# Performance work log

Measured on AMD Instinct MI355X. Metric: run time of the kernel, lower is better.

The kernel has to match this reference:

```python
import jax, jax.numpy as jnp
import numpy as np

D_MODEL = 256
N_HEADS = 4
WINDOW = 8
DECAY = 0.9
STEP_SIZE = 0.5


def _linear(x, w, b):
    # torch nn.Linear: y = x @ w.T + b, w: [out, in]
    return jnp.einsum('...i,oi->...o', x, w) + b


def _layernorm(x, scale, bias, eps=1e-5):
    mu = jnp.mean(x, axis=-1, keepdims=True)
    var = jnp.var(x, axis=-1, keepdims=True)
    return (x - mu) * jax.lax.rsqrt(var + eps) * scale + bias


def _ema(x, decay):
    # ema[t] = decay*ema[t-1] + (1-decay)*x[t], ema[-1]=0
    # (exactly the causal conv with weights (1-d)*d^i from the torch code)
    def step(c, xt):
        c = decay * c + (1.0 - decay) * xt
        return c, c
    _, ys = jax.lax.scan(step, jnp.zeros_like(x[:, 0]), jnp.swapaxes(x, 0, 1))
    return jnp.swapaxes(ys, 0, 1)


def setup_inputs() -> dict:
    key = jax.random.key(0)
    ks = iter(jax.random.split(key, 40))
    B, T, D = 8, 1024, D_MODEL
    s = 0.02
    inp = {
        'parallel_repr': jax.random.normal(next(ks), (B, T, D), jnp.float32),
        'sequential_state': jax.random.normal(next(ks), (B, D), jnp.float32),
        'trajectory_summary': jax.random.normal(next(ks), (B, D), jnp.float32),
        # MultiheadAttention params
        'in_proj_w': jax.random.normal(next(ks), (3 * D, D), jnp.float32) * s,
        'in_proj_b': jnp.zeros((3 * D,), jnp.float32),
        'out_proj_w': jax.random.normal(next(ks), (D, D), jnp.float32) * s,
        'out_proj_b': jnp.zeros((D,), jnp.float32),
        # depthwise causal conv (local history)
        'conv_w': jax.random.normal(next(ks), (D, 1, WINDOW), jnp.float32) * s,
        'conv_b': jnp.zeros((D,), jnp.float32),
        # parallel_to_sequential / sequential_to_parallel
        'p2s_w': jax.random.normal(next(ks), (D, D), jnp.float32) * s,
        'p2s_b': jnp.zeros((D,), jnp.float32),
        's2p_w': jax.random.normal(next(ks), (D, D), jnp.float32) * s,
        's2p_b': jnp.zeros((D,), jnp.float32),
        # transition MLP: 3D -> 2D -> D
        'trans_w1': jax.random.normal(next(ks), (2 * D, 3 * D), jnp.float32) * s,
        'trans_b1': jnp.zeros((2 * D,), jnp.float32),
        'trans_w2': jax.random.normal(next(ks), (D, 2 * D), jnp.float32) * s,
        'trans_b2': jnp.zeros((D,), jnp.float32),
        # FFN: D -> 4D -> D
        'ffn_w1': jax.random.normal(next(ks), (4 * D, D), jnp.float32) * s,
        'ffn_b1': jnp.zeros((4 * D,), jnp.float32),
        'ffn_w2': jax.random.normal(next(ks), (D, 4 * D), jnp.float32) * s,
        'ffn_b2': jnp.zeros((D,), jnp.float32),
        # LayerNorms
        'ln1_s': jnp.ones((D,), jnp.float32), 'ln1_b': jnp.zeros((D,), jnp.float32),
        'ln2_s': jnp.ones((D,), jnp.float32), 'ln2_b': jnp.zeros((D,), jnp.float32),
        'ln3_s': jnp.ones((D,), jnp.float32), 'ln3_b': jnp.zeros((D,), jnp.float32),
        'ln4_s': jnp.ones((D,), jnp.float32), 'ln4_b': jnp.zeros((D,), jnp.float32),
    }
    return inp


def _forward(parallel_repr, sequential_state,
             in_proj_w, in_proj_b, out_proj_w, out_proj_b,
             conv_w, conv_b, p2s_w, p2s_b, s2p_w, s2p_b,
             trans_w1, trans_b1, trans_w2, trans_b2,
             ffn_w1, ffn_b1, ffn_w2, ffn_b2,
             ln1_s, ln1_b, ln2_s, ln2_b, ln3_s, ln3_b, ln4_s, ln4_b):
    B, T, D = parallel_repr.shape
    H, hd = N_HEADS, D // N_HEADS

    # --- causal self-attention (nn.MultiheadAttention, batch_first) ---
    qkv = _linear(parallel_repr, in_proj_w, in_proj_b)
    q, k, v = jnp.split(qkv, 3, axis=-1)
    q = q.reshape(B, T, H, hd)
    k = k.reshape(B, T, H, hd)
    v = v.reshape(B, T, H, hd)
    scores = jnp.einsum('bqhd,bkhd->bhqk', q, k) / jnp.sqrt(jnp.asarray(hd, q.dtype))
    causal = jnp.triu(jnp.ones((T, T), bool), 1)
    scores = jnp.where(causal, jnp.finfo(scores.dtype).min, scores)
    attn = jax.nn.softmax(scores, axis=-1)
    attn_out = jnp.einsum('bhqk,bkhd->bqhd', attn, v).reshape(B, T, D)
    attn_out = _linear(attn_out, out_proj_w, out_proj_b)
    x = _layernorm(parallel_repr + attn_out, ln1_s, ln1_b)

    # --- depthwise causal conv (local history) ---
    xt = jnp.swapaxes(x, 1, 2)  # [B, D, T]
    xt_pad = jnp.pad(xt, ((0, 0), (0, 0), (WINDOW - 1, 0)))
    local = jax.lax.conv_general_dilated(
        xt_pad, conv_w, window_strides=(1,), padding='VALID',
        dimension_numbers=('NCH', 'OIH', 'NCH'), feature_group_count=D)
    local_history = jnp.swapaxes(local + conv_b[None, :, None], 1, 2)  # [B, T, D]

    # --- global EMA summary ---
    global_summary = _ema(x, DECAY)

    # --- transition deltas + cumsum state integration ---
    parallel_guidance = _linear(x, p2s_w, p2s_b)
    combined = jnp.concatenate([x + 0.3 * parallel_guidance, local_history, global_summary], axis=-1)
    h = jax.nn.gelu(_linear(combined, trans_w1, trans_b1), approximate=False)
    deltas = _linear(h, trans_w2, trans_b2)
    states = sequential_state[:, None, :] + jnp.cumsum(deltas, axis=1) * STEP_SIZE
    states = _layernorm(states, ln3_s, ln3_b)

    # --- FFN with sequential guidance ---
    seq_guidance = _linear(states, s2p_w, s2p_b)
    f = jax.nn.gelu(_linear(x + 0.3 * seq_guidance, ffn_w1, ffn_b1), approximate=False)
    ffn_out = _linear(f, ffn_w2, ffn_b2)
    x = _layernorm(x + ffn_out, ln2_s, ln2_b)

    final_sequential_state = _layernorm(states[:, -1, :], ln4_s, ln4_b)
    final_trajectory_summary = global_summary[:, -1, :]
    return x, final_sequential_state, final_trajectory_summary


def reference(parallel_repr, sequential_state, trajectory_summary,
              in_proj_w, in_proj_b, out_proj_w, out_proj_b,
              conv_w, conv_b, p2s_w, p2s_b, s2p_w, s2p_b,
              trans_w1, trans_b1, trans_w2, trans_b2,
              ffn_w1, ffn_b1, ffn_w2, ffn_b2,
              ln1_s, ln1_b, ln2_s, ln2_b, ln3_s, ln3_b, ln4_s, ln4_b):
    # trajectory_summary is accepted by the torch forward but never used.
    return _forward(parallel_repr, sequential_state,
                    in_proj_w, in_proj_b, out_proj_w, out_proj_b,
                    conv_w, conv_b, p2s_w, p2s_b, s2p_w, s2p_b,
                    trans_w1, trans_b1, trans_w2, trans_b2,
                    ffn_w1, ffn_b1, ffn_w2, ffn_b2,
                    ln1_s, ln1_b, ln2_s, ln2_b, ln3_s, ln3_b, ln4_s, ln4_b)
```

## Files before the change

kernel.cpp:

```cpp
#include <hip/hip_runtime.h>
#include <math.h>

typedef unsigned short u16;
typedef __attribute__((ext_vector_type(8))) short bf16x8;
typedef __attribute__((ext_vector_type(4))) float f32x4;

#define D_MODEL 256
#define T_SZ 1024
constexpr size_t S_ELT = (size_t)8192 * 256;
constexpr size_t MB = 1024 * 1024;

constexpr size_t OFF_QKV = 0;
constexpr size_t OFF_ATTN = 12 * MB;
constexpr size_t OFF_F = 0;
constexpr size_t OFF_X = 16 * MB;
constexpr size_t OFF_COMB = 24 * MB;
constexpr size_t OFF_FB = 36 * MB;
constexpr size_t OFF_H = 44 * MB;
constexpr size_t OFF_WB = 52 * MB;
constexpr size_t OFF_SCR1 = 55 * MB;
constexpr size_t OFF_SCR2 = 55 * MB + 262144;

constexpr int WB_INPROJ = 0;
constexpr int WB_OUTPROJ = 196608;
constexpr int WB_P2S = 262144;
constexpr int WB_S2P = 327680;
constexpr int WB_T1 = 393216;
constexpr int WB_T2 = 786432;
constexpr int WB_F1 = 917504;
constexpr int WB_F2 = 1179648;
constexpr int WB_TOTAL = 1441792;

__device__ __forceinline__ u16 f2bf(float f) {
  unsigned int u = __float_as_uint(f);
  u += 0x7fff + ((u >> 16) & 1);
  return (u16)(u >> 16);
}
__device__ __forceinline__ float bf2f(u16 s) {
  return __uint_as_float(((unsigned int)s) << 16);
}

__global__ __launch_bounds__(256)
void wconv_kernel(const float* w0, const float* w1, const float* w2,
                  const float* w3, const float* w4, const float* w5,
                  const float* w6, const float* w7, u16* __restrict__ outp) {
  const int idx4 = (blockIdx.x * 256 + threadIdx.x) * 4;
  if (idx4 >= WB_TOTAL) return;
  const int offs[9] = {WB_INPROJ, WB_OUTPROJ, WB_P2S,  WB_S2P, WB_T1,
                       WB_T2,     WB_F1,      WB_F2,   WB_TOTAL};
  const float* srcs[8] = {w0, w1, w2, w3, w4, w5, w6, w7};
  int seg = 0;
  while (idx4 >= offs[seg + 1]) ++seg;
  float4 v = *(const float4*)(srcs[seg] + (idx4 - offs[seg]));
  u16 o0 = f2bf(v.x), o1 = f2bf(v.y), o2 = f2bf(v.z), o3 = f2bf(v.w);
  unsigned int lo = (unsigned int)o0 | ((unsigned int)o1 << 16);
  unsigned int hi = (unsigned int)o2 | ((unsigned int)o3 << 16);
  uint2 pk = make_uint2(lo, hi);
  *(uint2*)(outp + idx4) = pk;
}

enum { EPI_NONE = 0, EPI_GELU = 1, EPI_ADDSCALE = 2 };

template <int EPI, int BN, bool OUTBF, bool AF32>
__global__ __launch_bounds__(256)
void mgemm(const void* __restrict__ Av, int lda,
           const u16* __restrict__ Wb, int K, const float* __restrict__ bias,
           void* __restrict__ Cv, int ldc, int col_off,
           const float* __restrict__ addsrc) {
  __shared__ u16 As[128][40];
  __shared__ u16 Bs[BN][40];
  const int tid = threadIdx.x;
  const int m0 = blockIdx.x * 128;
  const int n0 = blockIdx.y * BN;
  const int w = tid >> 6, lane = tid & 63;
  const int ln = lane & 15, quad = lane >> 4, kq8 = quad * 8;
  constexpr int MT = (BN == 128) ? 4 : 2;
  const int wm = (BN == 128) ? (w >> 1) * 64 : w * 32;
  const int wn = (BN == 128) ? (w & 1) * 64 : 0;

  f32x4 acc[MT][4] = {};

  const int srow = tid >> 2, skq = tid & 3;

  for (int k0 = 0; k0 < K; k0 += 32) {
    if (AF32) {
      const float* Af = (const float*)Av;
#pragma unroll
      for (int p = 0; p < 2; ++p) {
        const int row = srow + p * 64;
        const float* ap = Af + (size_t)(m0 + row) * lda + k0 + skq * 8;
        float4 v0 = *(const float4*)ap;
        float4 v1 = *(const float4*)(ap + 4);
        union { u16 h[8]; uint4 u; } pk;
        pk.h[0] = f2bf(v0.x); pk.h[1] = f2bf(v0.y);
        pk.h[2] = f2bf(v0.z); pk.h[3] = f2bf(v0.w);
        pk.h[4] = f2bf(v1.x); pk.h[5] = f2bf(v1.y);
        pk.h[6] = f2bf(v1.z); pk.h[7] = f2bf(v1.w);
        *(uint4*)&As[row][skq * 8] = pk.u;
      }
    } else {
      const u16* Ab = (const u16*)Av;
#pragma unroll
      for (int p = 0; p < 2; ++p) {
        const int row = srow + p * 64;
        *(uint4*)&As[row][skq * 8] =
            *(const uint4*)(Ab + (size_t)(m0 + row) * lda + k0 + skq * 8);
      }
    }
    *(uint4*)&Bs[srow][skq * 8] =
        *(const uint4*)(Wb + (size_t)(n0 + srow) * K + k0 + skq * 8);
    if (BN == 128) {
      *(uint4*)&Bs[srow + 64][skq * 8] =
          *(const uint4*)(Wb + (size_t)(n0 + srow + 64) * K + k0 + skq * 8);
    }
    __syncthreads();

    bf16x8 af[MT], bv[4];
#pragma unroll
    for (int i = 0; i < MT; ++i)
      af[i] = *(const bf16x8*)&As[wm + i * 16 + ln][kq8];
#pragma unroll
    for (int j = 0; j < 4; ++j)
      bv[j] = *(const bf16x8*)&Bs[wn + j * 16 + ln][kq8];
#pragma unroll
    for (int i = 0; i < MT; ++i)
#pragma unroll
      for (int j = 0; j < 4; ++j)
        acc[i][j] =
            __builtin_amdgcn_mfma_f32_16x16x32_bf16(af[i], bv[j], acc[i][j], 0, 0, 0);
    __syncthreads();
  }

#pragma unroll
  for (int i = 0; i < MT; ++i)
#pragma unroll
    for (int j = 0; j < 4; ++j) {
      const int col = n0 + wn + j * 16 + ln;
      const float bsv = bias[col];
#pragma unroll
      for (int r = 0; r < 4; ++r) {
        const int row = m0 + wm + i * 16 + quad * 4 + r;
        float v = acc[i][j][r] + bsv;
        if (EPI == EPI_GELU) v = 0.5f * v * (1.0f + erff(v * 0.70710678f));
        if (EPI == EPI_ADDSCALE) v = addsrc[(size_t)row * 256 + col] + 0.3f * v;
        if (OUTBF)
          ((u16*)Cv)[(size_t)row * ldc + col_off + col] = f2bf(v);
        else
          ((float*)Cv)[(size_t)row * ldc + col_off + col] = v;
      }
    }
}

__global__ __launch_bounds__(256)
void vtr_kernel(const u16* __restrict__ qkv, u16* __restrict__ vt) {
  __shared__ u16 Ls[64][66];
  const int tid = threadIdx.x;
  const int t0 = blockIdx.x * 64;
  const int bh = blockIdx.y;
  const int b = bh >> 2, h = bh & 3;
  const int r0 = tid >> 3, c8 = (tid & 7) * 8;
#pragma unroll
  for (int p = 0; p < 2; ++p) {
    const int t = t0 + r0 + p * 32;
    *(uint4*)&Ls[r0 + p * 32][c8] =
        *(const uint4*)(qkv + (size_t)(b * T_SZ + t) * 768 + 512 + h * 64 + c8);
  }
  __syncthreads();
#pragma unroll
  for (int p = 0; p < 2; ++p) {
    const int d = r0 + p * 32;
    union { u16 h16[8]; uint4 u; } pk;
#pragma unroll
    for (int e = 0; e < 8; ++e) pk.h16[e] = Ls[c8 + e][d];
    *(uint4*)(vt + (size_t)(bh * 64 + d) * T_SZ + t0 + c8) = pk.u;
  }
}

__global__ __launch_bounds__(256)
void attn_flash(const u16* __restrict__ qkv, const u16* __restrict__ vt,
                u16* __restrict__ outp) {
  __shared__ u16 Ps[4][16][72];
  const int tid = threadIdx.x;
  const int w = tid >> 6, lane = tid & 63;
  const int ln = lane & 15, quad = lane >> 4, kq8 = quad * 8;
  const int wu = blockIdx.x * 4 + w;
  const int bh = wu >> 6, s = wu & 63;
  const int qt = (s & 1) ? (63 - (s >> 1)) : (s >> 1);
  const int q0 = qt * 16;
  const int b = bh >> 2, h = bh & 3;
  const u16* base = qkv + (size_t)b * T_SZ * 768;
  const u16* vbase = vt + (size_t)bh * 64 * T_SZ;

  bf16x8 qf[2];
#pragma unroll
  for (int ks = 0; ks < 2; ++ks)
    qf[ks] = *(const bf16x8*)(base + (size_t)(q0 + ln) * 768 + h * 64 +
                              ks * 32 + kq8);
  const short ob = (short)0x3F80;
  const bf16x8 ones = {ob, ob, ob, ob, ob, ob, ob, ob};

  f32x4 O[4] = {};
  f32x4 l_acc = {};
  const int ntiles = (qt >> 2) + 1;
  for (int jt = 0; jt < ntiles; ++jt) {
    const int c0 = jt * 64;
    f32x4 sv[4] = {};
#pragma unroll
    for (int ks = 0; ks < 2; ++ks)
#pragma unroll
      for (int j = 0; j < 4; ++j) {
        bf16x8 kf = *(const bf16x8*)(base + (size_t)(c0 + j * 16 + ln) * 768 +
                                     256 + h * 64 + ks * 32 + kq8);
        sv[j] = __builtin_amdgcn_mfma_f32_16x16x32_bf16(qf[ks], kf, sv[j], 0, 0, 0);
      }
    const bool need_mask = (c0 + 63 > q0);
#pragma unroll
    for (int j = 0; j < 4; ++j)
#pragma unroll
      for (int r = 0; r < 4; ++r) {
        float p = __expf(sv[j][r] * 0.125f);
        if (need_mask && (c0 + j * 16 + ln > q0 + quad * 4 + r)) p = 0.f;
        Ps[w][quad * 4 + r][j * 16 + ln] = f2bf(p);
      }
#pragma unroll
    for (int ks = 0; ks < 2; ++ks) {
      bf16x8 pf = *(const bf16x8*)&Ps[w][ln][ks * 32 + kq8];
      l_acc = __builtin_amdgcn_mfma_f32_16x16x32_bf16(pf, ones, l_acc, 0, 0, 0);
#pragma unroll
      for (int j = 0; j < 4; ++j) {
        bf16x8 vf = *(const bf16x8*)(vbase + (size_t)(j * 16 + ln) * T_SZ +
                                     c0 + ks * 32 + kq8);
        O[j] = __builtin_amdgcn_mfma_f32_16x16x32_bf16(pf, vf, O[j], 0, 0, 0);
      }
    }
  }
  u16* op = outp + (size_t)b * T_SZ * 256;
#pragma unroll
  for (int r = 0; r < 4; ++r) {
    const float inv = 1.f / l_acc[r];
#pragma unroll
    for (int j = 0; j < 4; ++j)
      op[(size_t)(q0 + quad * 4 + r) * 256 + h * 64 + j * 16 + ln] =
          f2bf(O[j][r] * inv);
  }
}

__device__ __forceinline__ float block_reduce_sum(float v, float* tmp) {
#pragma unroll
  for (int o = 32; o > 0; o >>= 1) v += __shfl_down(v, o);
  const int lane = threadIdx.x & 63, wid = threadIdx.x >> 6;
  if (lane == 0) tmp[wid] = v;
  __syncthreads();
  v = tmp[0] + tmp[1] + tmp[2] + tmp[3];
  __syncthreads();
  return v;
}

__device__ __forceinline__ float ln_finish(float v, float s1, float s2,
                                           float g, float bb) {
  float mean = s1 * (1.f / 256.f);
  float var = s2 * (1.f / 256.f) - mean * mean;
  return (v - mean) * rsqrtf(var + 1e-5f) * g + bb;
}

__global__ __launch_bounds__(256)
void ln_add_kernel(const float* __restrict__ a, const float* __restrict__ addsrc,
                   const float* __restrict__ g, const float* __restrict__ bb,
                   float* __restrict__ outp) {
  __shared__ float tmp[4];
  const size_t row = blockIdx.x;
  const int d = threadIdx.x;
  float v = a[row * 256 + d] + addsrc[row * 256 + d];
  float s1 = block_reduce_sum(v, tmp);
  float s2 = block_reduce_sum(v * v, tmp);
  outp[row * 256 + d] = ln_finish(v, s1, s2, g[d], bb[d]);
}

__global__ __launch_bounds__(256)
void ln3_states_kernel(const float* __restrict__ deltas, const float* __restrict__ scr,
                       const float* __restrict__ seq, const float* __restrict__ g,
                       const float* __restrict__ bb, u16* __restrict__ st) {
  __shared__ float tmp[4];
  const int row = blockIdx.x;
  const int b = row >> 10, t = row & 1023;
  const int d = threadIdx.x;
  float v = seq[b * 256 + d] +
            0.5f * (deltas[(size_t)row * 256 + d] +
                    scr[(size_t)(b * 32 + (t >> 5)) * 256 + d]);
  float s1 = block_reduce_sum(v, tmp);
  float s2 = block_reduce_sum(v * v, tmp);
  st[(size_t)row * 256 + d] = f2bf(ln_finish(v, s1, s2, g[d], bb[d]));
}

__global__ __launch_bounds__(256)
void ln4_kernel(const u16* __restrict__ st, const float* __restrict__ g,
                const float* __restrict__ bb, float* __restrict__ outp) {
  __shared__ float tmp[4];
  const int b = blockIdx.x, d = threadIdx.x;
  float v = bf2f(st[(size_t)(b * T_SZ + 1023) * 256 + d]);
  float s1 = block_reduce_sum(v, tmp);
  float s2 = block_reduce_sum(v * v, tmp);
  outp[b * 256 + d] = ln_finish(v, s1, s2, g[d], bb[d]);
}

__global__ __launch_bounds__(256)
void emaconv_kernel(const float* __restrict__ x, const float* __restrict__ cw,
                    const float* __restrict__ cb, u16* __restrict__ comb,
                    float* __restrict__ scr) {
  const int bc = blockIdx.x;
  const int b = bc >> 5, ch = bc & 31;
  const int d = threadIdx.x;
  const int t0 = ch * 32;
  float wreg[8];
#pragma unroll
  for (int j = 0; j < 8; ++j) wreg[j] = cw[d * 8 + j];
  const float bias = cb[d];
  float xw[8];
#pragma unroll
  for (int j = 0; j < 7; ++j) {
    const int ts = t0 - 7 + j;
    xw[j] = (ts >= 0) ? x[(size_t)(b * T_SZ + ts) * 256 + d] : 0.f;
  }
  float c = 0.f;
#pragma unroll
  for (int tl = 0; tl < 32; ++tl) {
    const size_t row = (size_t)(b * T_SZ + t0 + tl);
    xw[7] = x[row * 256 + d];
    float conv = bias;
#pragma unroll
    for (int j = 0; j < 8; ++j) conv = fmaf(xw[j], wreg[j], conv);
    c = 0.9f * c + 0.1f * xw[7];
    comb[row * 768 + 256 + d] = f2bf(conv);
    comb[row * 768 + 512 + d] = f2bf(c);
#pragma unroll
    for (int j = 0; j < 7; ++j) xw[j] = xw[j + 1];
  }
  scr[(size_t)bc * 256 + d] = c;
}

__global__ __launch_bounds__(256)
void ema_b_kernel(float* __restrict__ scr) {
  const int b = blockIdx.x, d = threadIdx.x;
  const float q32 = 0.03433683820292512f;
  float carry = 0.f;
  for (int ch = 0; ch < 32; ++ch) {
    const size_t idx = (size_t)(b * 32 + ch) * 256 + d;
    float e = scr[idx];
    scr[idx] = carry;
    carry = e + q32 * carry;
  }
}

__global__ __launch_bounds__(256)
void ema_c_kernel(u16* __restrict__ comb, const float* __restrict__ scr,
                  float* __restrict__ fts) {
  const int row = blockIdx.x;
  const int b = row >> 10, t = row & 1023;
  const int d = threadIdx.x;
  const int ch = t >> 5, tl = t & 31;
  float carry = scr[(size_t)(b * 32 + ch) * 256 + d];
  float l = bf2f(comb[(size_t)row * 768 + 512 + d]);
  float y = fmaf(__powf(0.9f, (float)(tl + 1)), carry, l);
  comb[(size_t)row * 768 + 512 + d] = f2bf(y);
  if (t == 1023) fts[b * 256 + d] = y;
}

__global__ __launch_bounds__(256)
void cs_a_kernel(float* __restrict__ deltas, float* __restrict__ scr) {
  const int bc = blockIdx.x;
  const int b = bc >> 5, ch = bc & 31;
  const int d = threadIdx.x;
  const int t0 = ch * 32;
  float c = 0.f;
  for (int tl = 0; tl < 32; ++tl) {
    const size_t idx = (size_t)(b * T_SZ + t0 + tl) * 256 + d;
    c += deltas[idx];
    deltas[idx] = c;
  }
  scr[(size_t)bc * 256 + d] = c;
}

__global__ __launch_bounds__(256)
void cs_b_kernel(float* __restrict__ scr) {
  const int b = blockIdx.x, d = threadIdx.x;
  float carry = 0.f;
  for (int ch = 0; ch < 32; ++ch) {
    const size_t idx = (size_t)(b * 32 + ch) * 256 + d;
    float e = scr[idx];
    scr[idx] = carry;
    carry += e;
  }
}

extern "C" void kernel_launch(void* const* d_in, const int* in_sizes, int n_in,
                              void* d_out, int out_size, void* d_ws,
                              size_t ws_size, hipStream_t stream) {
  (void)in_sizes; (void)n_in; (void)out_size; (void)ws_size;
  const float* parallel_repr = (const float*)d_in[0];
  const float* sequential_state = (const float*)d_in[1];
  const float* in_proj_w = (const float*)d_in[3];
  const float* in_proj_b = (const float*)d_in[4];
  const float* out_proj_w = (const float*)d_in[5];
  const float* out_proj_b = (const float*)d_in[6];
  const float* conv_w = (const float*)d_in[7];
  const float* conv_b = (const float*)d_in[8];
  const float* p2s_w = (const float*)d_in[9];
  const float* p2s_b = (const float*)d_in[10];
  const float* s2p_w = (const float*)d_in[11];
  const float* s2p_b = (const float*)d_in[12];
  const float* trans_w1 = (const float*)d_in[13];
  const float* trans_b1 = (const float*)d_in[14];
  const float* trans_w2 = (const float*)d_in[15];
  const float* trans_b2 = (const float*)d_in[16];
  const float* ffn_w1 = (const float*)d_in[17];
  const float* ffn_b1 = (const float*)d_in[18];
  const float* ffn_w2 = (const float*)d_in[19];
  const float* ffn_b2 = (const float*)d_in[20];
  const float* ln1_s = (const float*)d_in[21];
  const float* ln1_b = (const float*)d_in[22];
  const float* ln2_s = (const float*)d_in[23];
  const float* ln2_b = (const float*)d_in[24];
  const float* ln3_s = (const float*)d_in[25];
  const float* ln3_b = (const float*)d_in[26];
  const float* ln4_s = (const float*)d_in[27];
  const float* ln4_b = (const float*)d_in[28];

  char* ws = (char*)d_ws;
  u16* qkv_bf = (u16*)(ws + OFF_QKV);
  u16* attn_bf = (u16*)(ws + OFF_ATTN);
  u16* states_bf = (u16*)(ws + OFF_ATTN);
  u16* f_bf = (u16*)(ws + OFF_F);
  float* x = (float*)(ws + OFF_X);
  u16* comb = (u16*)(ws + OFF_COMB);
  u16* ffn_in = (u16*)(ws + OFF_COMB);
  float* fbuf = (float*)(ws + OFF_FB);
  u16* vt = (u16*)(ws + OFF_H);
  u16* h_bf = (u16*)(ws + OFF_H);
  u16* wb = (u16*)(ws + OFF_WB);
  float* scr1 = (float*)(ws + OFF_SCR1);
  float* scr2 = (float*)(ws + OFF_SCR2);
  float* out = (float*)d_out;
  float* out_fss = out + S_ELT;
  float* out_fts = out + S_ELT + 2048;

  const dim3 blk(256);

  wconv_kernel<<<1408, blk, 0, stream>>>(in_proj_w, out_proj_w, p2s_w, s2p_w,
                                         trans_w1, trans_w2, ffn_w1, ffn_w2, wb);
  mgemm<EPI_NONE, 128, true, true><<<dim3(64, 6), blk, 0, stream>>>(
      parallel_repr, 256, wb + WB_INPROJ, 256, in_proj_b, qkv_bf, 768, 0, nullptr);
  vtr_kernel<<<dim3(16, 32), blk, 0, stream>>>(qkv_bf, vt);
  attn_flash<<<512, blk, 0, stream>>>(qkv_bf, vt, attn_bf);
  mgemm<EPI_NONE, 64, false, false><<<dim3(64, 4), blk, 0, stream>>>(
      attn_bf, 256, wb + WB_OUTPROJ, 256, out_proj_b, fbuf, 256, 0, nullptr);
  ln_add_kernel<<<8192, blk, 0, stream>>>(parallel_repr, fbuf, ln1_s, ln1_b, x);
  emaconv_kernel<<<256, blk, 0, stream>>>(x, conv_w, conv_b, comb, scr1);
  ema_b_kernel<<<8, blk, 0, stream>>>(scr1);
  ema_c_kernel<<<8192, blk, 0, stream>>>(comb, scr1, out_fts);
  mgemm<EPI_ADDSCALE, 64, true, true><<<dim3(64, 4), blk, 0, stream>>>(
      x, 256, wb + WB_P2S, 256, p2s_b, comb, 768, 0, x);
  mgemm<EPI_GELU, 128, true, false><<<dim3(64, 4), blk, 0, stream>>>(
      comb, 768, wb + WB_T1, 768, trans_b1, h_bf, 512, 0, nullptr);
  mgemm<EPI_NONE, 64, false, false><<<dim3(64, 4), blk, 0, stream>>>(
      h_bf, 512, wb + WB_T2, 512, trans_b2, fbuf, 256, 0, nullptr);
  cs_a_kernel<<<256, blk, 0, stream>>>(fbuf, scr2);
  cs_b_kernel<<<8, blk, 0, stream>>>(scr2);
  ln3_states_kernel<<<8192, blk, 0, stream>>>(fbuf, scr2, sequential_state,
                                              ln3_s, ln3_b, states_bf);
  ln4_kernel<<<8, blk, 0, stream>>>(states_bf, ln4_s, ln4_b, out_fss);
  mgemm<EPI_ADDSCALE, 64, true, false><<<dim3(64, 4), blk, 0, stream>>>(
      states_bf, 256, wb + WB_S2P, 256, s2p_b, ffn_in, 256, 0, x);
  mgemm<EPI_GELU, 128, true, false><<<dim3(64, 8), blk, 0, stream>>>(
      ffn_in, 256, wb + WB_F1, 256, ffn_b1, f_bf, 1024, 0, nullptr);
  mgemm<EPI_NONE, 64, false, false><<<dim3(64, 4), blk, 0, stream>>>(
      f_bf, 1024, wb + WB_F2, 1024, ffn_b2, fbuf, 256, 0, nullptr);
  ln_add_kernel<<<8192, blk, 0, stream>>>(x, fbuf, ln2_s, ln2_b, out);
}
```

Baseline: 316.4 us.

## Stage GEMM tiles via global_load_lds, pre-convert fp32 A operands, add BM=64 tiles

The GEMM now loads A and W tiles straight into LDS with the global_load_lds builtin, using an unpadded 16-row-group layout in place of register-staged padded copies. Fp32 A operands are dropped from the GEMM: parallel_repr is converted by a new cvtbf kernel, and the LN1 output is written a second time as bf16. N=256 GEMMs switch to 64x64 tiles to double the grid. This adds a conversion kernel and extra bf16 traffic, and the unpadded LDS layout may cause bank conflicts on the fragment reads.

```diff
diff --git a/kernel.cpp b/kernel.cpp
--- a/kernel.cpp
+++ b/kernel.cpp
@@ -17,6 +17,7 @@
 constexpr size_t OFF_COMB = 24 * MB;
 constexpr size_t OFF_FB = 36 * MB;
 constexpr size_t OFF_H = 44 * MB;
+constexpr size_t OFF_XBF = 48 * MB;
 constexpr size_t OFF_WB = 52 * MB;
 constexpr size_t OFF_SCR1 = 55 * MB;
 constexpr size_t OFF_SCR2 = 55 * MB + 262144;
@@ -38,6 +39,12 @@
 }
 __device__ __forceinline__ float bf2f(u16 s) {
   return __uint_as_float(((unsigned int)s) << 16);
+}
+
+__device__ __forceinline__ void glds16(const u16* g, u16* l) {
+  __builtin_amdgcn_global_load_lds(
+      (const __attribute__((address_space(1))) void*)g,
+      (__attribute__((address_space(3))) void*)l, 16, 0, 0);
 }
 
 __global__ __launch_bounds__(256)
@@ -52,76 +59,68 @@
   int seg = 0;
   while (idx4 >= offs[seg + 1]) ++seg;
   float4 v = *(const float4*)(srcs[seg] + (idx4 - offs[seg]));
-  u16 o0 = f2bf(v.x), o1 = f2bf(v.y), o2 = f2bf(v.z), o3 = f2bf(v.w);
-  unsigned int lo = (unsigned int)o0 | ((unsigned int)o1 << 16);
-  unsigned int hi = (unsigned int)o2 | ((unsigned int)o3 << 16);
-  uint2 pk = make_uint2(lo, hi);
-  *(uint2*)(outp + idx4) = pk;
+  unsigned int lo = (unsigned int)f2bf(v.x) | ((unsigned int)f2bf(v.y) << 16);
+  unsigned int hi = (unsigned int)f2bf(v.z) | ((unsigned int)f2bf(v.w) << 16);
+  *(uint2*)(outp + idx4) = make_uint2(lo, hi);
+}
+
+__global__ __launch_bounds__(256)
+void cvtbf_kernel(const float* __restrict__ src, u16* __restrict__ dst) {
+  const int i4 = (blockIdx.x * 256 + threadIdx.x) * 4;
+  float4 v = *(const float4*)(src + i4);
+  unsigned int lo = (unsigned int)f2bf(v.x) | ((unsigned int)f2bf(v.y) << 16);
+  unsigned int hi = (unsigned int)f2bf(v.z) | ((unsigned int)f2bf(v.w) << 16);
+  *(uint2*)(dst + i4) = make_uint2(lo, hi);
 }
 
 enum { EPI_NONE = 0, EPI_GELU = 1, EPI_ADDSCALE = 2 };
 
-template <int EPI, int BN, bool OUTBF, bool AF32>
-__global__ __launch_bounds__(256)
-void mgemm(const void* __restrict__ Av, int lda,
+template <int EPI, int BM, int BN, bool OUTBF>
+__global__ __launch_bounds__(256)
+void mgemm(const u16* __restrict__ A, int lda,
            const u16* __restrict__ Wb, int K, const float* __restrict__ bias,
            void* __restrict__ Cv, int ldc, int col_off,
            const float* __restrict__ addsrc) {
-  __shared__ u16 As[128][40];
-  __shared__ u16 Bs[BN][40];
+  __shared__ u16 As[BM * 32];
+  __shared__ u16 Bs[BN * 32];
   const int tid = threadIdx.x;
-  const int m0 = blockIdx.x * 128;
+  const int w = tid >> 6, lane = tid & 63;
+  const int ln = lane & 15, quad = lane >> 4;
+  const int m0 = blockIdx.x * BM;
   const int n0 = blockIdx.y * BN;
-  const int w = tid >> 6, lane = tid & 63;
-  const int ln = lane & 15, quad = lane >> 4, kq8 = quad * 8;
-  constexpr int MT = (BN == 128) ? 4 : 2;
-  const int wm = (BN == 128) ? (w >> 1) * 64 : w * 32;
-  const int wn = (BN == 128) ? (w & 1) * 64 : 0;
+  constexpr int MT = (BM == 128 && BN == 128) ? 4 : (BM == 128 ? 2 : 1);
+  const int wm = (BM == 128 && BN == 128) ? (w >> 1) * 64
+                 : (BM == 128)            ? w * 32
+                                          : w * 16;
+  const int wn = (BM == 128 && BN == 128) ? (w & 1) * 64 : 0;
+  constexpr int APW = BM / 64;
+  constexpr int BPW = BN / 64;
 
   f32x4 acc[MT][4] = {};
 
-  const int srow = tid >> 2, skq = tid & 3;
+  const int grow = lane >> 2;
+  const int gk8 = (lane & 3) * 8;
 
   for (int k0 = 0; k0 < K; k0 += 32) {
-    if (AF32) {
-      const float* Af = (const float*)Av;
-#pragma unroll
-      for (int p = 0; p < 2; ++p) {
-        const int row = srow + p * 64;
-        const float* ap = Af + (size_t)(m0 + row) * lda + k0 + skq * 8;
-        float4 v0 = *(const float4*)ap;
-        float4 v1 = *(const float4*)(ap + 4);
-        union { u16 h[8]; uint4 u; } pk;
-        pk.h[0] = f2bf(v0.x); pk.h[1] = f2bf(v0.y);
-        pk.h[2] = f2bf(v0.z); pk.h[3] = f2bf(v0.w);
-        pk.h[4] = f2bf(v1.x); pk.h[5] = f2bf(v1.y);
-        pk.h[6] = f2bf(v1.z); pk.h[7] = f2bf(v1.w);
-        *(uint4*)&As[row][skq * 8] = pk.u;
-      }
-    } else {
-      const u16* Ab = (const u16*)Av;
-#pragma unroll
-      for (int p = 0; p < 2; ++p) {
-        const int row = srow + p * 64;
-        *(uint4*)&As[row][skq * 8] =
-            *(const uint4*)(Ab + (size_t)(m0 + row) * lda + k0 + skq * 8);
-      }
+#pragma unroll
+    for (int p = 0; p < APW; ++p) {
+      const int g = w * APW + p;
+      glds16(A + (size_t)(m0 + g * 16 + grow) * lda + k0 + gk8, As + g * 512);
     }
-    *(uint4*)&Bs[srow][skq * 8] =
-        *(const uint4*)(Wb + (size_t)(n0 + srow) * K + k0 + skq * 8);
-    if (BN == 128) {
-      *(uint4*)&Bs[srow + 64][skq * 8] =
-          *(const uint4*)(Wb + (size_t)(n0 + srow + 64) * K + k0 + skq * 8);
+#pragma unroll
+    for (int p = 0; p < BPW; ++p) {
+      const int g = w * BPW + p;
+      glds16(Wb + (size_t)(n0 + g * 16 + grow) * K + k0 + gk8, Bs + g * 512);
     }
     __syncthreads();
 
+    const u16* abase = As + (wm >> 4) * 512 + ln * 32 + quad * 8;
+    const u16* bbase = Bs + (wn >> 4) * 512 + ln * 32 + quad * 8;
     bf16x8 af[MT], bv[4];
 #pragma unroll
-    for (int i = 0; i < MT; ++i)
-      af[i] = *(const bf16x8*)&As[wm + i * 16 + ln][kq8];
-#pragma unroll
-    for (int j = 0; j < 4; ++j)
-      bv[j] = *(const bf16x8*)&Bs[wn + j * 16 + ln][kq8];
+    for (int i = 0; i < MT; ++i) af[i] = *(const bf16x8*)(abase + i * 512);
+#pragma unroll
+    for (int j = 0; j < 4; ++j) bv[j] = *(const bf16x8*)(bbase + j * 512);
 #pragma unroll
     for (int i = 0; i < MT; ++i)
 #pragma unroll
@@ -266,14 +265,16 @@
 __global__ __launch_bounds__(256)
 void ln_add_kernel(const float* __restrict__ a, const float* __restrict__ addsrc,
                    const float* __restrict__ g, const float* __restrict__ bb,
-                   float* __restrict__ outp) {
+                   float* __restrict__ outp, u16* __restrict__ obf) {
   __shared__ float tmp[4];
   const size_t row = blockIdx.x;
   const int d = threadIdx.x;
   float v = a[row * 256 + d] + addsrc[row * 256 + d];
   float s1 = block_reduce_sum(v, tmp);
   float s2 = block_reduce_sum(v * v, tmp);
-  outp[row * 256 + d] = ln_finish(v, s1, s2, g[d], bb[d]);
+  float y = ln_finish(v, s1, s2, g[d], bb[d]);
+  outp[row * 256 + d] = y;
+  if (obf) obf[row * 256 + d] = f2bf(y);
 }
 
 __global__ __launch_bounds__(256)
@@ -398,23 +399,15 @@
   (void)in_sizes; (void)n_in; (void)out_size; (void)ws_size;
   const float* parallel_repr = (const float*)d_in[0];
   const float* sequential_state = (const float*)d_in[1];
-  const float* in_proj_w = (const float*)d_in[3];
   const float* in_proj_b = (const float*)d_in[4];
-  const float* out_proj_w = (const float*)d_in[5];
   const float* out_proj_b = (const float*)d_in[6];
   const float* conv_w = (const float*)d_in[7];
   const float* conv_b = (const float*)d_in[8];
-  const float* p2s_w = (const float*)d_in[9];
   const float* p2s_b = (const float*)d_in[10];
-  const float* s2p_w = (const float*)d_in[11];
   const float* s2p_b = (const float*)d_in[12];
-  const float* trans_w1 = (const float*)d_in[13];
   const float* trans_b1 = (const float*)d_in[14];
-  const float* trans_w2 = (const float*)d_in[15];
   const float* trans_b2 = (const float*)d_in[16];
-  const float* ffn_w1 = (const float*)d_in[17];
   const float* ffn_b1 = (const float*)d_in[18];
-  const float* ffn_w2 = (const float*)d_in[19];
   const float* ffn_b2 = (const float*)d_in[20];
   const float* ln1_s = (const float*)d_in[21];
   const float* ln1_b = (const float*)d_in[22];
@@ -432,10 +425,12 @@
   u16* f_bf = (u16*)(ws + OFF_F);
   float* x = (float*)(ws + OFF_X);
   u16* comb = (u16*)(ws + OFF_COMB);
+  u16* pr_bf = (u16*)(ws + OFF_COMB);
   u16* ffn_in = (u16*)(ws + OFF_COMB);
   float* fbuf = (float*)(ws + OFF_FB);
   u16* vt = (u16*)(ws + OFF_H);
   u16* h_bf = (u16*)(ws + OFF_H);
+  u16* x_bf = (u16*)(ws + OFF_XBF);
   u16* wb = (u16*)(ws + OFF_WB);
   float* scr1 = (float*)(ws + OFF_SCR1);
   float* scr2 = (float*)(ws + OFF_SCR2);
@@ -445,34 +440,38 @@
 
   const dim3 blk(256);
 
-  wconv_kernel<<<1408, blk, 0, stream>>>(in_proj_w, out_proj_w, p2s_w, s2p_w,
-                                         trans_w1, trans_w2, ffn_w1, ffn_w2, wb);
-  mgemm<EPI_NONE, 128, true, true><<<dim3(64, 6), blk, 0, stream>>>(
-      parallel_repr, 256, wb + WB_INPROJ, 256, in_proj_b, qkv_bf, 768, 0, nullptr);
+  wconv_kernel<<<1408, blk, 0, stream>>>(
+      (const float*)d_in[3], (const float*)d_in[5], (const float*)d_in[9],
+      (const float*)d_in[11], (const float*)d_in[13], (const float*)d_in[15],
+      (const float*)d_in[17], (const float*)d_in[19], wb);
+  cvtbf_kernel<<<2048, blk, 0, stream>>>(parallel_repr, pr_bf);
+  mgemm<EPI_NONE, 128, 128, true><<<dim3(64, 6), blk, 0, stream>>>(
+      pr_bf, 256, wb + WB_INPROJ, 256, in_proj_b, qkv_bf, 768, 0, nullptr);
   vtr_kernel<<<dim3(16, 32), blk, 0, stream>>>(qkv_bf, vt);
   attn_flash<<<512, blk, 0, stream>>>(qkv_bf, vt, attn_bf);
-  mgemm<EPI_NONE, 64, false, false><<<dim3(64, 4), blk, 0, stream>>>(
+  mgemm<EPI_NONE, 64, 64, false><<<dim3(128, 4), blk, 0, stream>>>(
       attn_bf, 256, wb + WB_OUTPROJ, 256, out_proj_b, fbuf, 256, 0, nullptr);
-  ln_add_kernel<<<8192, blk, 0, stream>>>(parallel_repr, fbuf, ln1_s, ln1_b, x);
+  ln_add_kernel<<<8192, blk, 0, stream>>>(parallel_repr, fbuf, ln1_s, ln1_b, x,
+                                          x_bf);
   emaconv_kernel<<<256, blk, 0, stream>>>(x, conv_w, conv_b, comb, scr1);
   ema_b_kernel<<<8, blk, 0, stream>>>(scr1);
   ema_c_kernel<<<8192, blk, 0, stream>>>(comb, scr1, out_fts);
-  mgemm<EPI_ADDSCALE, 64, true, true><<<dim3(64, 4), blk, 0, stream>>>(
-      x, 256, wb + WB_P2S, 256, p2s_b, comb, 768, 0, x);
-  mgemm<EPI_GELU, 128, true, false><<<dim3(64, 4), blk, 0, stream>>>(
+  mgemm<EPI_ADDSCALE, 64, 64, true><<<dim3(128, 4), blk, 0, stream>>>(
+      x_bf, 256, wb + WB_P2S, 256, p2s_b, comb, 768, 0, x);
+  mgemm<EPI_GELU, 128, 128, true><<<dim3(64, 4), blk, 0, stream>>>(
       comb, 768, wb + WB_T1, 768, trans_b1, h_bf, 512, 0, nullptr);
-  mgemm<EPI_NONE, 64, false, false><<<dim3(64, 4), blk, 0, stream>>>(
+  mgemm<EPI_NONE, 64, 64, false><<<dim3(128, 4), blk, 0, stream>>>(
       h_bf, 512, wb + WB_T2, 512, trans_b2, fbuf, 256, 0, nullptr);
   cs_a_kernel<<<256, blk, 0, stream>>>(fbuf, scr2);
   cs_b_kernel<<<8, blk, 0, stream>>>(scr2);
   ln3_states_kernel<<<8192, blk, 0, stream>>>(fbuf, scr2, sequential_state,
                                               ln3_s, ln3_b, states_bf);
   ln4_kernel<<<8, blk, 0, stream>>>(states_bf, ln4_s, ln4_b, out_fss);
-  mgemm<EPI_ADDSCALE, 64, true, false><<<dim3(64, 4), blk, 0, stream>>>(
+  mgemm<EPI_ADDSCALE, 64, 64, true><<<dim3(128, 4), blk, 0, stream>>>(
       states_bf, 256, wb + WB_S2P, 256, s2p_b, ffn_in, 256, 0, x);
-  mgemm<EPI_GELU, 128, true, false><<<dim3(64, 8), blk, 0, stream>>>(
+  mgemm<EPI_GELU, 128, 128, true><<<dim3(64, 8), blk, 0, stream>>>(
       ffn_in, 256, wb + WB_F1, 256, ffn_b1, f_bf, 1024, 0, nullptr);
-  mgemm<EPI_NONE, 64, false, false><<<dim3(64, 4), blk, 0, stream>>>(
+  mgemm<EPI_NONE, 64, 64, false><<<dim3(128, 4), blk, 0, stream>>>(
       f_bf, 1024, wb + WB_F2, 1024, ffn_b2, fbuf, 256, 0, nullptr);
-  ln_add_kernel<<<8192, blk, 0, stream>>>(x, fbuf, ln2_s, ln2_b, out);
-}
+  ln_add_kernel<<<8192, blk, 0, stream>>>(x, fbuf, ln2_s, ln2_b, out, nullptr);
+}
```

Result: faster. 303.3 us (-4.2%).
